# Kernel optimization log

Hardware: AMD Instinct MI355X
Metric: run time of the kernel (lower is better)

Reference implementation:

```python
import jax, jax.numpy as jnp
import numpy as np

# Event marker constants (PASS/MAP both trigger map writes, STEP triggers step writes)
PASS, MAP, STEP = 0, 1, 2
GRAPH_STEPS = 3
B, T, D, K, V = 64, 12, 256, 256, 512
S = 2 * K  # num_symbols


def gelu(x):
    return jax.nn.gelu(x, approximate=False)  # torch nn.GELU default = exact erf


def mlp2(x, W1, b1, W2, b2):
    return gelu(x @ W1 + b1) @ W2 + b2


def setup_inputs() -> dict:
    key = jax.random.key(0)
    ks = jax.random.split(key, 32)

    def lin(k, fan_in, shape):
        return (jax.random.normal(k, shape, dtype=jnp.float32) / np.float32(np.sqrt(fan_in)))

    return {
        "event_marker": jax.random.randint(ks[0], (B, T), 0, 3),
        "source_idx": jax.random.randint(ks[1], (B, T), 0, S),
        "source_valid": jax.random.randint(ks[2], (B, T), 0, 2),
        "target_symbol_idx": jax.random.randint(ks[3], (B, T), 0, S),
        "target_symbol_valid": jax.random.randint(ks[4], (B, T), 0, 2),
        "target_value_idx": jax.random.randint(ks[5], (B, T), 0, V),
        "target_value_valid": jax.random.randint(ks[6], (B, T), 0, 2),
        "query_idx": jax.random.randint(ks[7], (B,), 0, S),
        "query_valid": jax.random.randint(ks[8], (B,), 0, 2),
        "evidence": jax.random.normal(ks[9], (B, T, D), dtype=jnp.float32),
        "symbol_emb": jax.random.normal(ks[10], (S, D), dtype=jnp.float32) * 0.02,
        "value_emb": jax.random.normal(ks[11], (V, D), dtype=jnp.float32) * 0.02,
        "Wmg1": lin(ks[12], D, (D, D)), "bmg1": jnp.zeros((D,), jnp.float32),
        "Wmg2": lin(ks[13], D, (D, 1)), "bmg2": jnp.zeros((1,), jnp.float32),
        "Wsg1": lin(ks[14], D, (D, D)), "bsg1": jnp.zeros((D,), jnp.float32),
        "Wsg2": lin(ks[15], D, (D, 1)), "bsg2": jnp.zeros((1,), jnp.float32),
        "Wf1": lin(ks[16], 2 * D, (2 * D, D)), "bf1": jnp.zeros((D,), jnp.float32),
        "Wf2": lin(ks[17], D, (D, D)), "bf2": jnp.zeros((D,), jnp.float32),
        "Wo1": lin(ks[18], 2 * D, (2 * D, D)), "bo1": jnp.zeros((D,), jnp.float32),
        "Wo2": lin(ks[19], D, (D, V)), "bo2": jnp.zeros((V,), jnp.float32),
    }


def reference(event_marker, source_idx, source_valid, target_symbol_idx,
              target_symbol_valid, target_value_idx, target_value_valid,
              query_idx, query_valid, evidence, symbol_emb, value_emb,
              Wmg1, bmg1, Wmg2, bmg2, Wsg1, bsg1, Wsg2, bsg2,
              Wf1, bf1, Wf2, bf2, Wo1, bo1, Wo2, bo2):
    f32 = evidence.dtype
    brange = jnp.arange(B)

    # --- TypedGraphMemory.update, applied over T sequential events ---
    # one-hot outer-product write  ==  scatter-add of gated scalar at (b, src, tgt)
    def step(carry, ev):
        map_mem, step_mem = carry
        marker, src, sv, tsym, tsv, tval, tvv, evd = ev
        mg = jax.nn.sigmoid(mlp2(evd, Wmg1, bmg1, Wmg2, bmg2))[:, 0]  # [B]
        sg = jax.nn.sigmoid(mlp2(evd, Wsg1, bsg1, Wsg2, bsg2))[:, 0]  # [B]
        map_mask = (((marker == PASS) | (marker == MAP)) & (sv > 0) & (tvv > 0)).astype(f32)
        step_mask = ((marker == STEP) & (sv > 0) & (tsv > 0)).astype(f32)
        src_c = jnp.clip(src, 0, S - 1)
        tsym_c = jnp.clip(tsym, 0, S - 1)
        tval_c = jnp.clip(tval, 0, V - 1)
        map_mem = map_mem.at[brange, src_c, tval_c].add(mg * map_mask)
        step_mem = step_mem.at[brange, src_c, tsym_c].add(sg * step_mask)
        return (map_mem, step_mem), None

    ev_seq = (event_marker.T, source_idx.T, source_valid.T, target_symbol_idx.T,
              target_symbol_valid.T, target_value_idx.T, target_value_valid.T,
              jnp.swapaxes(evidence, 0, 1))  # time-major
    init = (jnp.zeros((B, S, V), f32), jnp.zeros((B, S, S), f32))
    (map_mem, step_mem), _ = jax.lax.scan(step, init, ev_seq)

    # --- TypedGraphMemory.query_readout ---
    walk = jax.nn.one_hot(jnp.clip(query_idx, 0, S - 1), S, dtype=f32)
    walk = walk * query_valid.astype(f32)[:, None]
    acc_v = jnp.einsum('bs,bsv->bv', walk, map_mem)   # [B,V]
    acc_s = walk @ symbol_emb                         # [B,D]
    for _ in range(GRAPH_STEPS):
        walk = jnp.einsum('bs,bst->bt', walk, step_mem)
        acc_v = acc_v + jnp.einsum('bs,bsv->bv', walk, map_mem)
        acc_s = acc_s + walk @ symbol_emb
    graph_state = jnp.concatenate([acc_s, acc_v @ value_emb], axis=-1)  # [B,2D]
    logits = mlp2(graph_state, Wo1, bo1, Wo2, bo2)      # [B,V]
    feedback = mlp2(graph_state, Wf1, bf1, Wf2, bf2)    # [B,D]
    return logits, feedback
```

## Files before the change

### kernel.cpp

```cpp
#include <hip/hip_runtime.h>
#include <math.h>

#define NB 64
#define NT 12
#define ND 256
#define NS 512
#define NV 512

__device__ float g_gates[2 * NB * NT];
__device__ float g_gs[NB * 512];
__device__ float g_H[2 * NB * 256];

__device__ __forceinline__ float gelu_exact(float x) {
    return 0.5f * x * (1.0f + erff(x * 0.70710678118654752f));
}
__device__ __forceinline__ float sigmoidf_(float x) {
    return 1.0f / (1.0f + __expf(-x));
}

__global__ __launch_bounds__(1024) void k_gates(
    const float* __restrict__ evidence,
    const float* __restrict__ Wmg1, const float* __restrict__ bmg1,
    const float* __restrict__ Wmg2, const float* __restrict__ bmg2,
    const float* __restrict__ Wsg1, const float* __restrict__ bsg1,
    const float* __restrict__ Wsg2, const float* __restrict__ bsg2)
{
    const int blk = blockIdx.x;
    const int b  = blk >> 2;
    const int g  = (blk >> 1) & 1;
    const int th = blk & 1;
    const int t0 = th * 6;
    const int tid = threadIdx.x;
    const int j = tid & 255;
    const int ih = tid >> 8;
    const int lane = tid & 63, wv = tid >> 6;

    __shared__ float part[3][6][256];
    __shared__ float red[4][6];

    const float* __restrict__ W1 = g ? Wsg1 : Wmg1;
    const float* __restrict__ b1 = g ? bsg1 : bmg1;
    const float* __restrict__ W2 = g ? Wsg2 : Wmg2;
    const float* __restrict__ b2 = g ? bsg2 : bmg2;
    const float* __restrict__ ev = evidence + b * (NT * ND) + t0 * ND;

    float h[6];
    #pragma unroll
    for (int t = 0; t < 6; ++t) h[t] = 0.0f;

    const int ibase = ih * 64;
    #pragma unroll 8
    for (int ii = 0; ii < 64; ++ii) {
        const int i = ibase + ii;
        float w = W1[i * ND + j];
        #pragma unroll
        for (int t = 0; t < 6; ++t) h[t] += ev[t * ND + i] * w;
    }

    if (ih > 0) {
        #pragma unroll
        for (int t = 0; t < 6; ++t) part[ih - 1][t][j] = h[t];
    }
    __syncthreads();
    if (ih == 0) {
        const float b1j = b1[j], w2j = W2[j];
        #pragma unroll
        for (int t = 0; t < 6; ++t) {
            float v = gelu_exact(h[t] + part[0][t][j] + part[1][t][j] +
                                 part[2][t][j] + b1j) * w2j;
            #pragma unroll
            for (int off = 32; off > 0; off >>= 1) v += __shfl_down(v, off, 64);
            if (lane == 0) red[wv][t] = v;
        }
    }
    __syncthreads();
    if (tid < 6) {
        float s = red[0][tid] + red[1][tid] + red[2][tid] + red[3][tid] + b2[0];
        g_gates[g * (NB * NT) + b * NT + t0 + tid] = sigmoidf_(s);
    }
}

__global__ __launch_bounds__(512) void k_readout(
    const int* __restrict__ marker, const int* __restrict__ srci,
    const int* __restrict__ srcv, const int* __restrict__ tsymi,
    const int* __restrict__ tsymv, const int* __restrict__ tvali,
    const int* __restrict__ tvalv, const int* __restrict__ qidx,
    const int* __restrict__ qvld,
    const float* __restrict__ symbol_emb, const float* __restrict__ value_emb)
{
    const int b = blockIdx.x, tid = threadIdx.x;
    __shared__ float walk[NS], nxt[NS];
    __shared__ int   esrc[NT], etsym[NT], etval[NT];
    __shared__ float mapw[NT], stepw[NT];
    __shared__ int   sidx[64]; __shared__ float sval[64];
    __shared__ int   vidx[64]; __shared__ float vval[64];
    __shared__ int   scnt, vcnt;

    walk[tid] = 0.f; nxt[tid] = 0.f;
    if (tid == 0) { scnt = 0; vcnt = 0; }
    if (tid < NT) {
        int e = b * NT + tid;
        int mk = marker[e];
        int sv_ = srcv[e], tsv_ = tsymv[e], tvv_ = tvalv[e];
        esrc[tid]  = min(max(srci[e], 0), NS - 1);
        etsym[tid] = min(max(tsymi[e], 0), NS - 1);
        etval[tid] = min(max(tvali[e], 0), NV - 1);
        bool mmask = ((mk == 0) || (mk == 1)) && (sv_ > 0) && (tvv_ > 0);
        bool smask = (mk == 2) && (sv_ > 0) && (tsv_ > 0);
        mapw[tid]  = mmask ? g_gates[0 * (NB * NT) + e] : 0.f;
        stepw[tid] = smask ? g_gates[1 * (NB * NT) + e] : 0.f;
    }
    __syncthreads();
    if (tid == 0) {
        int qc = min(max(qidx[b], 0), NS - 1);
        float qv = (float)qvld[b];
        walk[qc] = qv;
        if (qv != 0.f) { sidx[0] = qc; sval[0] = qv; scnt = 1; }
    }
    __syncthreads();
    if (tid < NT) {
        float c = walk[esrc[tid]] * mapw[tid];
        if (c != 0.f) { int k = atomicAdd(&vcnt, 1); vidx[k] = etval[tid]; vval[k] = c; }
    }
    __syncthreads();
    for (int stp = 0; stp < 3; ++stp) {
        if (tid < NT) {
            float c = walk[esrc[tid]] * stepw[tid];
            if (c != 0.f) {
                atomicAdd(&nxt[etsym[tid]], c);
                int k = atomicAdd(&scnt, 1); sidx[k] = etsym[tid]; sval[k] = c;
            }
        }
        __syncthreads();
        { float a = nxt[tid]; walk[tid] = a; nxt[tid] = 0.f; }
        __syncthreads();
        if (tid < NT) {
            float c = walk[esrc[tid]] * mapw[tid];
            if (c != 0.f) { int k = atomicAdd(&vcnt, 1); vidx[k] = etval[tid]; vval[k] = c; }
        }
        __syncthreads();
    }
    const int d = tid & 255;
    const float* __restrict__ emb  = (tid < 256) ? symbol_emb : value_emb;
    const int*   idxl = (tid < 256) ? sidx : vidx;
    const float* vall = (tid < 256) ? sval : vval;
    const int n = (tid < 256) ? scnt : vcnt;
    float acc = 0.f;
    int k = 0;
    for (; k + 4 <= n; k += 4) {
        int   i0 = idxl[k],     i1 = idxl[k + 1], i2 = idxl[k + 2], i3 = idxl[k + 3];
        float w0 = vall[k],     w1 = vall[k + 1], w2 = vall[k + 2], w3 = vall[k + 3];
        float r0 = emb[i0 * ND + d], r1 = emb[i1 * ND + d];
        float r2 = emb[i2 * ND + d], r3 = emb[i3 * ND + d];
        acc += w0 * r0; acc += w1 * r1; acc += w2 * r2; acc += w3 * r3;
    }
    for (; k < n; ++k) acc += vall[k] * emb[idxl[k] * ND + d];
    g_gs[b * 512 + (tid < 256 ? 0 : 256) + d] = acc;
}

__global__ __launch_bounds__(512) void k_mlp1(
    const float* __restrict__ Wo1, const float* __restrict__ bo1,
    const float* __restrict__ Wf1, const float* __restrict__ bf1)
{
    const int blk = blockIdx.x;
    const int m = blk >> 5;
    const int r = blk & 31;
    const int js = r >> 3, bt = r & 7;
    const int tid = threadIdx.x;
    const int lane = tid & 63;
    const int bsub = (tid >> 6) & 3;
    const int ih = tid >> 8;
    const int j = js * 64 + lane;
    const int b0 = bt * 8 + bsub * 2, b1_ = b0 + 1;

    const float* __restrict__ W1   = (m ? Wf1 : Wo1) + ih * 256 * 256;
    const float* __restrict__ bias = m ? bf1 : bo1;
    const float* __restrict__ x0 = g_gs + b0 * 512 + ih * 256;
    const float* __restrict__ x1 = g_gs + b1_ * 512 + ih * 256;

    float a0 = 0.f, a1 = 0.f;
    #pragma unroll 8
    for (int i = 0; i < 256; ++i) {
        float w = W1[i * 256 + j];
        a0 += x0[i] * w; a1 += x1[i] * w;
    }
    __shared__ float part[256][2];
    if (ih == 1) { part[tid & 255][0] = a0; part[tid & 255][1] = a1; }
    __syncthreads();
    if (ih == 0) {
        float bj = bias[j];
        g_H[m * (NB * 256) + b0 * 256 + j]  = gelu_exact(a0 + part[tid][0] + bj);
        g_H[m * (NB * 256) + b1_ * 256 + j] = gelu_exact(a1 + part[tid][1] + bj);
    }
}

__global__ __launch_bounds__(512) void k_mlp2(
    const float* __restrict__ Wo2, const float* __restrict__ bo2,
    const float* __restrict__ Wf2, const float* __restrict__ bf2,
    float* __restrict__ out)
{
    const int blk = blockIdx.x;
    const int tid = threadIdx.x;
    const int lane = tid & 63;
    const int bsub = (tid >> 6) & 3;
    const int ih = tid >> 8;
    __shared__ float part[256][2];

    if (blk < 64) {
        const int bt = blk >> 3, vs = blk & 7;
        const int v = vs * 64 + lane;
        const int b0 = bt * 8 + bsub * 2, b1_ = b0 + 1;
        const float* __restrict__ h0 = g_H + b0 * 256 + ih * 128;
        const float* __restrict__ h1 = g_H + b1_ * 256 + ih * 128;
        const float* __restrict__ Wp = Wo2 + ih * 128 * 512;
        float a0 = 0.f, a1 = 0.f;
        #pragma unroll 8
        for (int k = 0; k < 128; ++k) {
            float w = Wp[k * 512 + v];
            a0 += h0[k] * w; a1 += h1[k] * w;
        }
        if (ih == 1) { part[tid & 255][0] = a0; part[tid & 255][1] = a1; }
        __syncthreads();
        if (ih == 0) {
            float bv = bo2[v];
            out[b0 * 512 + v]  = a0 + part[tid][0] + bv;
            out[b1_ * 512 + v] = a1 + part[tid][1] + bv;
        }
    } else {
        const int r = blk - 64;
        const int bt = r >> 2, ds = r & 3;
        const int d = ds * 64 + lane;
        const int b0 = bt * 8 + bsub * 2, b1_ = b0 + 1;
        const float* __restrict__ h0 = g_H + (NB * 256) + b0 * 256 + ih * 128;
        const float* __restrict__ h1 = g_H + (NB * 256) + b1_ * 256 + ih * 128;
        const float* __restrict__ Wp = Wf2 + ih * 128 * 256;
        float a0 = 0.f, a1 = 0.f;
        #pragma unroll 8
        for (int k = 0; k < 128; ++k) {
            float w = Wp[k * 256 + d];
            a0 += h0[k] * w; a1 += h1[k] * w;
        }
        if (ih == 1) { part[tid & 255][0] = a0; part[tid & 255][1] = a1; }
        __syncthreads();
        if (ih == 0) {
            float bd = bf2[d];
            out[NB * NV + b0 * 256 + d]  = a0 + part[tid][0] + bd;
            out[NB * NV + b1_ * 256 + d] = a1 + part[tid][1] + bd;
        }
    }
}

extern "C" void kernel_launch(void* const* d_in, const int* in_sizes, int n_in,
                              void* d_out, int out_size, void* d_ws, size_t ws_size,
                              hipStream_t stream) {
    const int* event_marker       = (const int*)d_in[0];
    const int* source_idx         = (const int*)d_in[1];
    const int* source_valid       = (const int*)d_in[2];
    const int* target_symbol_idx  = (const int*)d_in[3];
    const int* target_symbol_vld  = (const int*)d_in[4];
    const int* target_value_idx   = (const int*)d_in[5];
    const int* target_value_vld   = (const int*)d_in[6];
    const int* query_idx          = (const int*)d_in[7];
    const int* query_valid        = (const int*)d_in[8];
    const float* evidence   = (const float*)d_in[9];
    const float* symbol_emb = (const float*)d_in[10];
    const float* value_emb  = (const float*)d_in[11];
    const float* Wmg1 = (const float*)d_in[12]; const float* bmg1 = (const float*)d_in[13];
    const float* Wmg2 = (const float*)d_in[14]; const float* bmg2 = (const float*)d_in[15];
    const float* Wsg1 = (const float*)d_in[16]; const float* bsg1 = (const float*)d_in[17];
    const float* Wsg2 = (const float*)d_in[18]; const float* bsg2 = (const float*)d_in[19];
    const float* Wf1  = (const float*)d_in[20]; const float* bf1  = (const float*)d_in[21];
    const float* Wf2  = (const float*)d_in[22]; const float* bf2  = (const float*)d_in[23];
    const float* Wo1  = (const float*)d_in[24]; const float* bo1  = (const float*)d_in[25];
    const float* Wo2  = (const float*)d_in[26]; const float* bo2  = (const float*)d_in[27];

    (void)d_ws; (void)ws_size;

    k_gates<<<dim3(256), dim3(1024), 0, stream>>>(
        evidence, Wmg1, bmg1, Wmg2, bmg2, Wsg1, bsg1, Wsg2, bsg2);
    k_readout<<<dim3(64), dim3(512), 0, stream>>>(
        event_marker, source_idx, source_valid, target_symbol_idx,
        target_symbol_vld, target_value_idx, target_value_vld,
        query_idx, query_valid, symbol_emb, value_emb);
    k_mlp1<<<dim3(64), dim3(512), 0, stream>>>(Wo1, bo1, Wf1, bf1);
    k_mlp2<<<dim3(96), dim3(512), 0, stream>>>(Wo2, bo2, Wf2, bf2, (float*)d_out);
}
```

Before: 155.9 us.

## Fuse gate, readout and MLP kernels into one persistent kernel with grid barriers

Merges the four sequential launches (gates, graph readout, MLP layer 1, MLP layer 2) into a single 256-block kernel. The stages are separated by software grid barriers built on global atomic counters and generation flags. Blocks not needed for later stages arrive at the first barrier and exit. The aim is to remove inter-kernel launch gaps and drains. In exchange it adds spin-wait barrier overhead and under-uses 1024-thread blocks in the later stages. It also depends on all 256 blocks being co-resident to avoid deadlock.

```diff
diff --git a/kernel.cpp b/kernel.cpp
--- a/kernel.cpp
+++ b/kernel.cpp
@@ -11,6 +11,9 @@
 __device__ float g_gs[NB * 512];
 __device__ float g_H[2 * NB * 256];
 
+__device__ unsigned g_cnt[3];
+__device__ unsigned g_gen[3];
+
 __device__ __forceinline__ float gelu_exact(float x) {
     return 0.5f * x * (1.0f + erff(x * 0.70710678118654752f));
 }
@@ -18,234 +21,267 @@
     return 1.0f / (1.0f + __expf(-x));
 }
 
-__global__ __launch_bounds__(1024) void k_gates(
-    const float* __restrict__ evidence,
-    const float* __restrict__ Wmg1, const float* __restrict__ bmg1,
-    const float* __restrict__ Wmg2, const float* __restrict__ bmg2,
-    const float* __restrict__ Wsg1, const float* __restrict__ bsg1,
-    const float* __restrict__ Wsg2, const float* __restrict__ bsg2)
-{
-    const int blk = blockIdx.x;
-    const int b  = blk >> 2;
-    const int g  = (blk >> 1) & 1;
-    const int th = blk & 1;
-    const int t0 = th * 6;
-    const int tid = threadIdx.x;
-    const int j = tid & 255;
-    const int ih = tid >> 8;
-    const int lane = tid & 63, wv = tid >> 6;
-
-    __shared__ float part[3][6][256];
-    __shared__ float red[4][6];
-
-    const float* __restrict__ W1 = g ? Wsg1 : Wmg1;
-    const float* __restrict__ b1 = g ? bsg1 : bmg1;
-    const float* __restrict__ W2 = g ? Wsg2 : Wmg2;
-    const float* __restrict__ b2 = g ? bsg2 : bmg2;
-    const float* __restrict__ ev = evidence + b * (NT * ND) + t0 * ND;
-
-    float h[6];
-    #pragma unroll
-    for (int t = 0; t < 6; ++t) h[t] = 0.0f;
-
-    const int ibase = ih * 64;
-    #pragma unroll 8
-    for (int ii = 0; ii < 64; ++ii) {
-        const int i = ibase + ii;
-        float w = W1[i * ND + j];
-        #pragma unroll
-        for (int t = 0; t < 6; ++t) h[t] += ev[t * ND + i] * w;
-    }
-
-    if (ih > 0) {
-        #pragma unroll
-        for (int t = 0; t < 6; ++t) part[ih - 1][t][j] = h[t];
+__device__ __forceinline__ void grid_bar(int idx, unsigned n, bool wait) {
+    __syncthreads();
+    if (threadIdx.x == 0) {
+        __threadfence();
+        unsigned g0 = __hip_atomic_load(&g_gen[idx], __ATOMIC_RELAXED,
+                                        __HIP_MEMORY_SCOPE_AGENT);
+        unsigned old = __hip_atomic_fetch_add(&g_cnt[idx], 1u,
+                                              __ATOMIC_ACQ_REL,
+                                              __HIP_MEMORY_SCOPE_AGENT);
+        if (old == n - 1u) {
+            __hip_atomic_store(&g_cnt[idx], 0u, __ATOMIC_RELAXED,
+                               __HIP_MEMORY_SCOPE_AGENT);
+            __hip_atomic_fetch_add(&g_gen[idx], 1u, __ATOMIC_RELEASE,
+                                   __HIP_MEMORY_SCOPE_AGENT);
+        } else if (wait) {
+            while (__hip_atomic_load(&g_gen[idx], __ATOMIC_RELAXED,
+                                     __HIP_MEMORY_SCOPE_AGENT) == g0)
+                __builtin_amdgcn_s_sleep(1);
+        }
+        __threadfence();
     }
     __syncthreads();
-    if (ih == 0) {
-        const float b1j = b1[j], w2j = W2[j];
-        #pragma unroll
-        for (int t = 0; t < 6; ++t) {
-            float v = gelu_exact(h[t] + part[0][t][j] + part[1][t][j] +
-                                 part[2][t][j] + b1j) * w2j;
-            #pragma unroll
-            for (int off = 32; off > 0; off >>= 1) v += __shfl_down(v, off, 64);
-            if (lane == 0) red[wv][t] = v;
-        }
-    }
-    __syncthreads();
-    if (tid < 6) {
-        float s = red[0][tid] + red[1][tid] + red[2][tid] + red[3][tid] + b2[0];
-        g_gates[g * (NB * NT) + b * NT + t0 + tid] = sigmoidf_(s);
-    }
-}
-
-__global__ __launch_bounds__(512) void k_readout(
+}
+
+__global__ __launch_bounds__(1024) void k_fused(
     const int* __restrict__ marker, const int* __restrict__ srci,
     const int* __restrict__ srcv, const int* __restrict__ tsymi,
     const int* __restrict__ tsymv, const int* __restrict__ tvali,
     const int* __restrict__ tvalv, const int* __restrict__ qidx,
     const int* __restrict__ qvld,
-    const float* __restrict__ symbol_emb, const float* __restrict__ value_emb)
+    const float* __restrict__ evidence,
+    const float* __restrict__ symbol_emb, const float* __restrict__ value_emb,
+    const float* __restrict__ Wmg1, const float* __restrict__ bmg1,
+    const float* __restrict__ Wmg2, const float* __restrict__ bmg2,
+    const float* __restrict__ Wsg1, const float* __restrict__ bsg1,
+    const float* __restrict__ Wsg2, const float* __restrict__ bsg2,
+    const float* __restrict__ Wf1, const float* __restrict__ bf1,
+    const float* __restrict__ Wf2, const float* __restrict__ bf2,
+    const float* __restrict__ Wo1, const float* __restrict__ bo1,
+    const float* __restrict__ Wo2, const float* __restrict__ bo2,
+    float* __restrict__ out)
 {
-    const int b = blockIdx.x, tid = threadIdx.x;
+    const int blk = blockIdx.x;
+    const int tid = threadIdx.x;
+
+    __shared__ float part1[3][6][256];
+    __shared__ float red[4][6];
     __shared__ float walk[NS], nxt[NS];
     __shared__ int   esrc[NT], etsym[NT], etval[NT];
     __shared__ float mapw[NT], stepw[NT];
     __shared__ int   sidx[64]; __shared__ float sval[64];
     __shared__ int   vidx[64]; __shared__ float vval[64];
     __shared__ int   scnt, vcnt;
-
-    walk[tid] = 0.f; nxt[tid] = 0.f;
-    if (tid == 0) { scnt = 0; vcnt = 0; }
-    if (tid < NT) {
-        int e = b * NT + tid;
-        int mk = marker[e];
-        int sv_ = srcv[e], tsv_ = tsymv[e], tvv_ = tvalv[e];
-        esrc[tid]  = min(max(srci[e], 0), NS - 1);
-        etsym[tid] = min(max(tsymi[e], 0), NS - 1);
-        etval[tid] = min(max(tvali[e], 0), NV - 1);
-        bool mmask = ((mk == 0) || (mk == 1)) && (sv_ > 0) && (tvv_ > 0);
-        bool smask = (mk == 2) && (sv_ > 0) && (tsv_ > 0);
-        mapw[tid]  = mmask ? g_gates[0 * (NB * NT) + e] : 0.f;
-        stepw[tid] = smask ? g_gates[1 * (NB * NT) + e] : 0.f;
+    __shared__ float part2[256][2];
+
+    {
+        const int b  = blk >> 2;
+        const int g  = (blk >> 1) & 1;
+        const int th = blk & 1;
+        const int t0 = th * 6;
+        const int j = tid & 255;
+        const int ih = tid >> 8;
+        const int lane = tid & 63, wv = tid >> 6;
+
+        const float* __restrict__ W1 = g ? Wsg1 : Wmg1;
+        const float* __restrict__ b1 = g ? bsg1 : bmg1;
+        const float* __restrict__ W2 = g ? Wsg2 : Wmg2;
+        const float* __restrict__ b2 = g ? bsg2 : bmg2;
+        const float* __restrict__ ev = evidence + b * (NT * ND) + t0 * ND;
+
+        float h[6];
+        #pragma unroll
+        for (int t = 0; t < 6; ++t) h[t] = 0.0f;
+
+        const int ibase = ih * 64;
+        #pragma unroll 8
+        for (int ii = 0; ii < 64; ++ii) {
+            const int i = ibase + ii;
+            float w = W1[i * ND + j];
+            #pragma unroll
+            for (int t = 0; t < 6; ++t) h[t] += ev[t * ND + i] * w;
+        }
+
+        if (ih > 0) {
+            #pragma unroll
+            for (int t = 0; t < 6; ++t) part1[ih - 1][t][j] = h[t];
+        }
+        __syncthreads();
+        if (ih == 0) {
+            const float b1j = b1[j], w2j = W2[j];
+            #pragma unroll
+            for (int t = 0; t < 6; ++t) {
+                float v = gelu_exact(h[t] + part1[0][t][j] + part1[1][t][j] +
+                                     part1[2][t][j] + b1j) * w2j;
+                #pragma unroll
+                for (int off = 32; off > 0; off >>= 1) v += __shfl_down(v, off, 64);
+                if (lane == 0) red[wv][t] = v;
+            }
+        }
+        __syncthreads();
+        if (tid < 6) {
+            float s = red[0][tid] + red[1][tid] + red[2][tid] + red[3][tid] + b2[0];
+            g_gates[g * (NB * NT) + b * NT + t0 + tid] = sigmoidf_(s);
+        }
     }
-    __syncthreads();
-    if (tid == 0) {
-        int qc = min(max(qidx[b], 0), NS - 1);
-        float qv = (float)qvld[b];
-        walk[qc] = qv;
-        if (qv != 0.f) { sidx[0] = qc; sval[0] = qv; scnt = 1; }
-    }
-    __syncthreads();
-    if (tid < NT) {
-        float c = walk[esrc[tid]] * mapw[tid];
-        if (c != 0.f) { int k = atomicAdd(&vcnt, 1); vidx[k] = etval[tid]; vval[k] = c; }
-    }
-    __syncthreads();
-    for (int stp = 0; stp < 3; ++stp) {
+
+    grid_bar(0, 256, blk < 96);
+    if (blk >= 96) return;
+
+    if (blk < 64) {
+        const int b = blk;
+        const bool a5 = (tid < 512);
+        if (a5) { walk[tid] = 0.f; nxt[tid] = 0.f; }
+        if (tid == 0) { scnt = 0; vcnt = 0; }
         if (tid < NT) {
-            float c = walk[esrc[tid]] * stepw[tid];
-            if (c != 0.f) {
-                atomicAdd(&nxt[etsym[tid]], c);
-                int k = atomicAdd(&scnt, 1); sidx[k] = etsym[tid]; sval[k] = c;
-            }
-        }
-        __syncthreads();
-        { float a = nxt[tid]; walk[tid] = a; nxt[tid] = 0.f; }
+            int e = b * NT + tid;
+            int mk = marker[e];
+            int sv_ = srcv[e], tsv_ = tsymv[e], tvv_ = tvalv[e];
+            esrc[tid]  = min(max(srci[e], 0), NS - 1);
+            etsym[tid] = min(max(tsymi[e], 0), NS - 1);
+            etval[tid] = min(max(tvali[e], 0), NV - 1);
+            bool mmask = ((mk == 0) || (mk == 1)) && (sv_ > 0) && (tvv_ > 0);
+            bool smask = (mk == 2) && (sv_ > 0) && (tsv_ > 0);
+            mapw[tid]  = mmask ? g_gates[0 * (NB * NT) + e] : 0.f;
+            stepw[tid] = smask ? g_gates[1 * (NB * NT) + e] : 0.f;
+        }
+        __syncthreads();
+        if (tid == 0) {
+            int qc = min(max(qidx[b], 0), NS - 1);
+            float qv = (float)qvld[b];
+            walk[qc] = qv;
+            if (qv != 0.f) { sidx[0] = qc; sval[0] = qv; scnt = 1; }
+        }
         __syncthreads();
         if (tid < NT) {
             float c = walk[esrc[tid]] * mapw[tid];
             if (c != 0.f) { int k = atomicAdd(&vcnt, 1); vidx[k] = etval[tid]; vval[k] = c; }
         }
         __syncthreads();
+        for (int stp = 0; stp < 3; ++stp) {
+            if (tid < NT) {
+                float c = walk[esrc[tid]] * stepw[tid];
+                if (c != 0.f) {
+                    atomicAdd(&nxt[etsym[tid]], c);
+                    int k = atomicAdd(&scnt, 1); sidx[k] = etsym[tid]; sval[k] = c;
+                }
+            }
+            __syncthreads();
+            if (a5) { float a = nxt[tid]; walk[tid] = a; nxt[tid] = 0.f; }
+            __syncthreads();
+            if (tid < NT) {
+                float c = walk[esrc[tid]] * mapw[tid];
+                if (c != 0.f) { int k = atomicAdd(&vcnt, 1); vidx[k] = etval[tid]; vval[k] = c; }
+            }
+            __syncthreads();
+        }
+        if (a5) {
+            const int d = tid & 255;
+            const float* __restrict__ emb  = (tid < 256) ? symbol_emb : value_emb;
+            const int*   idxl = (tid < 256) ? sidx : vidx;
+            const float* vall = (tid < 256) ? sval : vval;
+            const int n = (tid < 256) ? scnt : vcnt;
+            float acc = 0.f;
+            int k = 0;
+            for (; k + 4 <= n; k += 4) {
+                int   i0 = idxl[k],     i1 = idxl[k + 1], i2 = idxl[k + 2], i3 = idxl[k + 3];
+                float w0 = vall[k],     w1 = vall[k + 1], w2 = vall[k + 2], w3 = vall[k + 3];
+                float r0 = emb[i0 * ND + d], r1 = emb[i1 * ND + d];
+                float r2 = emb[i2 * ND + d], r3 = emb[i3 * ND + d];
+                acc += w0 * r0; acc += w1 * r1; acc += w2 * r2; acc += w3 * r3;
+            }
+            for (; k < n; ++k) acc += vall[k] * emb[idxl[k] * ND + d];
+            g_gs[b * 512 + (tid < 256 ? 0 : 256) + d] = acc;
+        }
+
+        grid_bar(1, 64, true);
+
+        {
+            const int m = blk >> 5;
+            const int r = blk & 31;
+            const int js = r >> 3, bt = r & 7;
+            const int lane = tid & 63;
+            const int bsub = (tid >> 6) & 3;
+            const int ih = tid >> 8;
+            const int j = js * 64 + lane;
+            const int b0 = bt * 8 + bsub * 2, b1_ = b0 + 1;
+
+            float a0 = 0.f, a1 = 0.f;
+            if (tid < 512) {
+                const float* __restrict__ W1 = (m ? Wf1 : Wo1) + ih * 256 * 256;
+                const float* __restrict__ x0 = g_gs + b0 * 512 + ih * 256;
+                const float* __restrict__ x1 = g_gs + b1_ * 512 + ih * 256;
+                #pragma unroll 8
+                for (int i = 0; i < 256; ++i) {
+                    float w = W1[i * 256 + j];
+                    a0 += x0[i] * w; a1 += x1[i] * w;
+                }
+            }
+            if (ih == 1) { part2[tid & 255][0] = a0; part2[tid & 255][1] = a1; }
+            __syncthreads();
+            if (ih == 0) {
+                const float* __restrict__ bias = m ? bf1 : bo1;
+                float bj = bias[j];
+                g_H[m * (NB * 256) + b0 * 256 + j]  = gelu_exact(a0 + part2[tid][0] + bj);
+                g_H[m * (NB * 256) + b1_ * 256 + j] = gelu_exact(a1 + part2[tid][1] + bj);
+            }
+        }
     }
-    const int d = tid & 255;
-    const float* __restrict__ emb  = (tid < 256) ? symbol_emb : value_emb;
-    const int*   idxl = (tid < 256) ? sidx : vidx;
-    const float* vall = (tid < 256) ? sval : vval;
-    const int n = (tid < 256) ? scnt : vcnt;
-    float acc = 0.f;
-    int k = 0;
-    for (; k + 4 <= n; k += 4) {
-        int   i0 = idxl[k],     i1 = idxl[k + 1], i2 = idxl[k + 2], i3 = idxl[k + 3];
-        float w0 = vall[k],     w1 = vall[k + 1], w2 = vall[k + 2], w3 = vall[k + 3];
-        float r0 = emb[i0 * ND + d], r1 = emb[i1 * ND + d];
-        float r2 = emb[i2 * ND + d], r3 = emb[i3 * ND + d];
-        acc += w0 * r0; acc += w1 * r1; acc += w2 * r2; acc += w3 * r3;
-    }
-    for (; k < n; ++k) acc += vall[k] * emb[idxl[k] * ND + d];
-    g_gs[b * 512 + (tid < 256 ? 0 : 256) + d] = acc;
-}
-
-__global__ __launch_bounds__(512) void k_mlp1(
-    const float* __restrict__ Wo1, const float* __restrict__ bo1,
-    const float* __restrict__ Wf1, const float* __restrict__ bf1)
-{
-    const int blk = blockIdx.x;
-    const int m = blk >> 5;
-    const int r = blk & 31;
-    const int js = r >> 3, bt = r & 7;
-    const int tid = threadIdx.x;
-    const int lane = tid & 63;
-    const int bsub = (tid >> 6) & 3;
-    const int ih = tid >> 8;
-    const int j = js * 64 + lane;
-    const int b0 = bt * 8 + bsub * 2, b1_ = b0 + 1;
-
-    const float* __restrict__ W1   = (m ? Wf1 : Wo1) + ih * 256 * 256;
-    const float* __restrict__ bias = m ? bf1 : bo1;
-    const float* __restrict__ x0 = g_gs + b0 * 512 + ih * 256;
-    const float* __restrict__ x1 = g_gs + b1_ * 512 + ih * 256;
-
-    float a0 = 0.f, a1 = 0.f;
-    #pragma unroll 8
-    for (int i = 0; i < 256; ++i) {
-        float w = W1[i * 256 + j];
-        a0 += x0[i] * w; a1 += x1[i] * w;
-    }
-    __shared__ float part[256][2];
-    if (ih == 1) { part[tid & 255][0] = a0; part[tid & 255][1] = a1; }
-    __syncthreads();
-    if (ih == 0) {
-        float bj = bias[j];
-        g_H[m * (NB * 256) + b0 * 256 + j]  = gelu_exact(a0 + part[tid][0] + bj);
-        g_H[m * (NB * 256) + b1_ * 256 + j] = gelu_exact(a1 + part[tid][1] + bj);
-    }
-}
-
-__global__ __launch_bounds__(512) void k_mlp2(
-    const float* __restrict__ Wo2, const float* __restrict__ bo2,
-    const float* __restrict__ Wf2, const float* __restrict__ bf2,
-    float* __restrict__ out)
-{
-    const int blk = blockIdx.x;
-    const int tid = threadIdx.x;
-    const int lane = tid & 63;
-    const int bsub = (tid >> 6) & 3;
-    const int ih = tid >> 8;
-    __shared__ float part[256][2];
-
-    if (blk < 64) {
-        const int bt = blk >> 3, vs = blk & 7;
-        const int v = vs * 64 + lane;
-        const int b0 = bt * 8 + bsub * 2, b1_ = b0 + 1;
-        const float* __restrict__ h0 = g_H + b0 * 256 + ih * 128;
-        const float* __restrict__ h1 = g_H + b1_ * 256 + ih * 128;
-        const float* __restrict__ Wp = Wo2 + ih * 128 * 512;
-        float a0 = 0.f, a1 = 0.f;
-        #pragma unroll 8
-        for (int k = 0; k < 128; ++k) {
-            float w = Wp[k * 512 + v];
-            a0 += h0[k] * w; a1 += h1[k] * w;
-        }
-        if (ih == 1) { part[tid & 255][0] = a0; part[tid & 255][1] = a1; }
-        __syncthreads();
-        if (ih == 0) {
-            float bv = bo2[v];
-            out[b0 * 512 + v]  = a0 + part[tid][0] + bv;
-            out[b1_ * 512 + v] = a1 + part[tid][1] + bv;
-        }
-    } else {
-        const int r = blk - 64;
-        const int bt = r >> 2, ds = r & 3;
-        const int d = ds * 64 + lane;
-        const int b0 = bt * 8 + bsub * 2, b1_ = b0 + 1;
-        const float* __restrict__ h0 = g_H + (NB * 256) + b0 * 256 + ih * 128;
-        const float* __restrict__ h1 = g_H + (NB * 256) + b1_ * 256 + ih * 128;
-        const float* __restrict__ Wp = Wf2 + ih * 128 * 256;
-        float a0 = 0.f, a1 = 0.f;
-        #pragma unroll 8
-        for (int k = 0; k < 128; ++k) {
-            float w = Wp[k * 256 + d];
-            a0 += h0[k] * w; a1 += h1[k] * w;
-        }
-        if (ih == 1) { part[tid & 255][0] = a0; part[tid & 255][1] = a1; }
-        __syncthreads();
-        if (ih == 0) {
-            float bd = bf2[d];
-            out[NB * NV + b0 * 256 + d]  = a0 + part[tid][0] + bd;
-            out[NB * NV + b1_ * 256 + d] = a1 + part[tid][1] + bd;
+
+    grid_bar(2, 96, true);
+
+    {
+        const int lane = tid & 63;
+        const int bsub = (tid >> 6) & 3;
+        const int ih = tid >> 8;
+
+        if (blk < 64) {
+            const int bt = blk >> 3, vs = blk & 7;
+            const int v = vs * 64 + lane;
+            const int b0 = bt * 8 + bsub * 2, b1_ = b0 + 1;
+            float a0 = 0.f, a1 = 0.f;
+            if (tid < 512) {
+                const float* __restrict__ h0 = g_H + b0 * 256 + ih * 128;
+                const float* __restrict__ h1 = g_H + b1_ * 256 + ih * 128;
+                const float* __restrict__ Wp = Wo2 + ih * 128 * 512;
+                #pragma unroll 8
+                for (int k = 0; k < 128; ++k) {
+                    float w = Wp[k * 512 + v];
+                    a0 += h0[k] * w; a1 += h1[k] * w;
+                }
+            }
+            if (ih == 1) { part2[tid & 255][0] = a0; part2[tid & 255][1] = a1; }
+            __syncthreads();
+            if (ih == 0) {
+                float bv = bo2[v];
+                out[b0 * 512 + v]  = a0 + part2[tid][0] + bv;
+                out[b1_ * 512 + v] = a1 + part2[tid][1] + bv;
+            }
+        } else {
+            const int r = blk - 64;
+            const int bt = r >> 2, ds = r & 3;
+            const int d = ds * 64 + lane;
+            const int b0 = bt * 8 + bsub * 2, b1_ = b0 + 1;
+            float a0 = 0.f, a1 = 0.f;
+            if (tid < 512) {
+                const float* __restrict__ h0 = g_H + (NB * 256) + b0 * 256 + ih * 128;
+                const float* __restrict__ h1 = g_H + (NB * 256) + b1_ * 256 + ih * 128;
+                const float* __restrict__ Wp = Wf2 + ih * 128 * 256;
+                #pragma unroll 8
+                for (int k = 0; k < 128; ++k) {
+                    float w = Wp[k * 256 + d];
+                    a0 += h0[k] * w; a1 += h1[k] * w;
+                }
+            }
+            if (ih == 1) { part2[tid & 255][0] = a0; part2[tid & 255][1] = a1; }
+            __syncthreads();
+            if (ih == 0) {
+                float bd = bf2[d];
+                out[NB * NV + b0 * 256 + d]  = a0 + part2[tid][0] + bd;
+                out[NB * NV + b1_ * 256 + d] = a1 + part2[tid][1] + bd;
+            }
         }
     }
 }
@@ -276,12 +312,10 @@
 
     (void)d_ws; (void)ws_size;
 
-    k_gates<<<dim3(256), dim3(1024), 0, stream>>>(
-        evidence, Wmg1, bmg1, Wmg2, bmg2, Wsg1, bsg1, Wsg2, bsg2);
-    k_readout<<<dim3(64), dim3(512), 0, stream>>>(
+    k_fused<<<dim3(256), dim3(1024), 0, stream>>>(
         event_marker, source_idx, source_valid, target_symbol_idx,
         target_symbol_vld, target_value_idx, target_value_vld,
-        query_idx, query_valid, symbol_emb, value_emb);
-    k_mlp1<<<dim3(64), dim3(512), 0, stream>>>(Wo1, bo1, Wf1, bf1);
-    k_mlp2<<<dim3(96), dim3(512), 0, stream>>>(Wo2, bo2, Wf2, bf2, (float*)d_out);
-}
+        query_idx, query_valid, evidence, symbol_emb, value_emb,
+        Wmg1, bmg1, Wmg2, bmg2, Wsg1, bsg1, Wsg2, bsg2,
+        Wf1, bf1, Wf2, bf2, Wo1, bo1, Wo2, bo2, (float*)d_out);
+}
```

New measurement: 174.0 us. +11.6%, slower.

## Repartition MLP kernels with 8-way K split to fill more CUs

Applied to the files above, without the earlier changes.

The first MLP layer kernel now launches 256 blocks, each handling two batch rows over 64 output columns. The K reduction is split across 8 wavefronts and summed through shared memory, replacing the old 2-way split. The second layer uses 192 blocks, each computing four batch rows per thread with an 8-way K split. The aim is more parallelism on the many-CU GPU and shorter serial dot-product loops, at the cost of more redundant weight reads across blocks and a larger shared-memory reduction.

```diff
diff --git a/kernel.cpp b/kernel.cpp
--- a/kernel.cpp
+++ b/kernel.cpp
@@ -163,34 +163,42 @@
     const float* __restrict__ Wf1, const float* __restrict__ bf1)
 {
     const int blk = blockIdx.x;
-    const int m = blk >> 5;
-    const int r = blk & 31;
-    const int js = r >> 3, bt = r & 7;
+    const int m  = blk >> 7;
+    const int r  = blk & 127;
+    const int js = r >> 5;
+    const int bp = r & 31;
     const int tid = threadIdx.x;
     const int lane = tid & 63;
-    const int bsub = (tid >> 6) & 3;
-    const int ih = tid >> 8;
+    const int oct = tid >> 6;
     const int j = js * 64 + lane;
-    const int b0 = bt * 8 + bsub * 2, b1_ = b0 + 1;
-
-    const float* __restrict__ W1   = (m ? Wf1 : Wo1) + ih * 256 * 256;
-    const float* __restrict__ bias = m ? bf1 : bo1;
-    const float* __restrict__ x0 = g_gs + b0 * 512 + ih * 256;
-    const float* __restrict__ x1 = g_gs + b1_ * 512 + ih * 256;
+    const int b0 = bp * 2, b1_ = b0 + 1;
+
+    const float* __restrict__ W1 = m ? Wf1 : Wo1;
+    const float* __restrict__ x0 = g_gs + b0 * 512;
+    const float* __restrict__ x1 = g_gs + b1_ * 512;
 
     float a0 = 0.f, a1 = 0.f;
+    const int i0 = oct * 64;
     #pragma unroll 8
-    for (int i = 0; i < 256; ++i) {
+    for (int ii = 0; ii < 64; ++ii) {
+        const int i = i0 + ii;
         float w = W1[i * 256 + j];
         a0 += x0[i] * w; a1 += x1[i] * w;
     }
-    __shared__ float part[256][2];
-    if (ih == 1) { part[tid & 255][0] = a0; part[tid & 255][1] = a1; }
-    __syncthreads();
-    if (ih == 0) {
+    __shared__ float2 part[8][64];
+    part[oct][lane] = make_float2(a0, a1);
+    __syncthreads();
+    if (oct == 0) {
+        const float* __restrict__ bias = m ? bf1 : bo1;
         float bj = bias[j];
-        g_H[m * (NB * 256) + b0 * 256 + j]  = gelu_exact(a0 + part[tid][0] + bj);
-        g_H[m * (NB * 256) + b1_ * 256 + j] = gelu_exact(a1 + part[tid][1] + bj);
+        float s0 = 0.f, s1 = 0.f;
+        #pragma unroll
+        for (int q = 0; q < 8; ++q) {
+            float2 p = part[q][lane];
+            s0 += p.x; s1 += p.y;
+        }
+        g_H[m * (NB * 256) + b0 * 256 + j]  = gelu_exact(s0 + bj);
+        g_H[m * (NB * 256) + b1_ * 256 + j] = gelu_exact(s1 + bj);
     }
 }
 
@@ -202,50 +210,71 @@
     const int blk = blockIdx.x;
     const int tid = threadIdx.x;
     const int lane = tid & 63;
-    const int bsub = (tid >> 6) & 3;
-    const int ih = tid >> 8;
-    __shared__ float part[256][2];
-
-    if (blk < 64) {
-        const int bt = blk >> 3, vs = blk & 7;
+    const int oct = tid >> 6;
+    __shared__ float4 part[8][64];
+
+    if (blk < 128) {
+        const int vs = blk >> 4, bt = blk & 15;
         const int v = vs * 64 + lane;
-        const int b0 = bt * 8 + bsub * 2, b1_ = b0 + 1;
-        const float* __restrict__ h0 = g_H + b0 * 256 + ih * 128;
-        const float* __restrict__ h1 = g_H + b1_ * 256 + ih * 128;
-        const float* __restrict__ Wp = Wo2 + ih * 128 * 512;
-        float a0 = 0.f, a1 = 0.f;
+        const int bb = bt * 4;
+        const float* __restrict__ h0 = g_H + (bb + 0) * 256;
+        const float* __restrict__ h1 = g_H + (bb + 1) * 256;
+        const float* __restrict__ h2 = g_H + (bb + 2) * 256;
+        const float* __restrict__ h3 = g_H + (bb + 3) * 256;
+        float a0 = 0.f, a1 = 0.f, a2 = 0.f, a3 = 0.f;
+        const int k0 = oct * 32;
         #pragma unroll 8
-        for (int k = 0; k < 128; ++k) {
-            float w = Wp[k * 512 + v];
-            a0 += h0[k] * w; a1 += h1[k] * w;
-        }
-        if (ih == 1) { part[tid & 255][0] = a0; part[tid & 255][1] = a1; }
-        __syncthreads();
-        if (ih == 0) {
+        for (int kk = 0; kk < 32; ++kk) {
+            const int k = k0 + kk;
+            float w = Wo2[k * 512 + v];
+            a0 += h0[k] * w; a1 += h1[k] * w; a2 += h2[k] * w; a3 += h3[k] * w;
+        }
+        part[oct][lane] = make_float4(a0, a1, a2, a3);
+        __syncthreads();
+        if (oct == 0) {
             float bv = bo2[v];
-            out[b0 * 512 + v]  = a0 + part[tid][0] + bv;
-            out[b1_ * 512 + v] = a1 + part[tid][1] + bv;
+            float s0 = 0.f, s1 = 0.f, s2 = 0.f, s3 = 0.f;
+            #pragma unroll
+            for (int q = 0; q < 8; ++q) {
+                float4 p = part[q][lane];
+                s0 += p.x; s1 += p.y; s2 += p.z; s3 += p.w;
+            }
+            out[(bb + 0) * 512 + v] = s0 + bv;
+            out[(bb + 1) * 512 + v] = s1 + bv;
+            out[(bb + 2) * 512 + v] = s2 + bv;
+            out[(bb + 3) * 512 + v] = s3 + bv;
         }
     } else {
-        const int r = blk - 64;
-        const int bt = r >> 2, ds = r & 3;
+        const int r = blk - 128;
+        const int ds = r >> 4, bt = r & 15;
         const int d = ds * 64 + lane;
-        const int b0 = bt * 8 + bsub * 2, b1_ = b0 + 1;
-        const float* __restrict__ h0 = g_H + (NB * 256) + b0 * 256 + ih * 128;
-        const float* __restrict__ h1 = g_H + (NB * 256) + b1_ * 256 + ih * 128;
-        const float* __restrict__ Wp = Wf2 + ih * 128 * 256;
-        float a0 = 0.f, a1 = 0.f;
+        const int bb = bt * 4;
+        const float* __restrict__ h0 = g_H + (NB * 256) + (bb + 0) * 256;
+        const float* __restrict__ h1 = g_H + (NB * 256) + (bb + 1) * 256;
+        const float* __restrict__ h2 = g_H + (NB * 256) + (bb + 2) * 256;
+        const float* __restrict__ h3 = g_H + (NB * 256) + (bb + 3) * 256;
+        float a0 = 0.f, a1 = 0.f, a2 = 0.f, a3 = 0.f;
+        const int k0 = oct * 32;
         #pragma unroll 8
-        for (int k = 0; k < 128; ++k) {
-            float w = Wp[k * 256 + d];
-            a0 += h0[k] * w; a1 += h1[k] * w;
-        }
-        if (ih == 1) { part[tid & 255][0] = a0; part[tid & 255][1] = a1; }
-        __syncthreads();
-        if (ih == 0) {
+        for (int kk = 0; kk < 32; ++kk) {
+            const int k = k0 + kk;
+            float w = Wf2[k * 256 + d];
+            a0 += h0[k] * w; a1 += h1[k] * w; a2 += h2[k] * w; a3 += h3[k] * w;
+        }
+        part[oct][lane] = make_float4(a0, a1, a2, a3);
+        __syncthreads();
+        if (oct == 0) {
             float bd = bf2[d];
-            out[NB * NV + b0 * 256 + d]  = a0 + part[tid][0] + bd;
-            out[NB * NV + b1_ * 256 + d] = a1 + part[tid][1] + bd;
+            float s0 = 0.f, s1 = 0.f, s2 = 0.f, s3 = 0.f;
+            #pragma unroll
+            for (int q = 0; q < 8; ++q) {
+                float4 p = part[q][lane];
+                s0 += p.x; s1 += p.y; s2 += p.z; s3 += p.w;
+            }
+            out[NB * NV + (bb + 0) * 256 + d] = s0 + bd;
+            out[NB * NV + (bb + 1) * 256 + d] = s1 + bd;
+            out[NB * NV + (bb + 2) * 256 + d] = s2 + bd;
+            out[NB * NV + (bb + 3) * 256 + d] = s3 + bd;
         }
     }
 }
@@ -282,6 +311,6 @@
         event_marker, source_idx, source_valid, target_symbol_idx,
         target_symbol_vld, target_value_idx, target_value_vld,
         query_idx, query_valid, symbol_emb, value_emb);
-    k_mlp1<<<dim3(64), dim3(512), 0, stream>>>(Wo1, bo1, Wf1, bf1);
-    k_mlp2<<<dim3(96), dim3(512), 0, stream>>>(Wo2, bo2, Wf2, bf2, (float*)d_out);
-}
+    k_mlp1<<<dim3(256), dim3(512), 0, stream>>>(Wo1, bo1, Wf1, bf1);
+    k_mlp2<<<dim3(192), dim3(512), 0, stream>>>(Wo2, bo2, Wf2, bf2, (float*)d_out);
+}
```

Measured after the change: 140.6 us. 1.11x faster.
